# Optimization experiments

Hardware: AMD Instinct MI355X
Metric: run time of the kernel (lower is better)

## Reference

```python
import jax, jax.numpy as jnp
import numpy as np

B, L, D = 2048, 64, 128
NODES = 512
EPS = 1e-6


def setup_inputs() -> dict:
    key = jax.random.key(0)
    ks = jax.random.split(key, 9)
    src_ids = jax.random.randint(ks[0], (B, L), 0, NODES, dtype=jnp.int32)
    dst_ids = jax.random.randint(ks[1], (B, L), 0, NODES, dtype=jnp.int32)
    src_node_ids = jax.random.randint(ks[2], (B,), 1, NODES, dtype=jnp.int32)
    dst_node_ids = jax.random.randint(ks[3], (B,), 1, NODES, dtype=jnp.int32)
    node_interact_times = 100.0 + jax.random.uniform(ks[4], (B,), jnp.float32)
    src_times = jax.random.uniform(ks[5], (B, L), jnp.float32) * 100.0
    dst_times = jax.random.uniform(ks[6], (B, L), jnp.float32) * 100.0
    W1 = jax.random.normal(ks[7], (1, D), jnp.float32) * 0.5
    b1 = jnp.zeros((D,), jnp.float32)
    W2 = jax.random.normal(ks[8], (D, D), jnp.float32) * (1.0 / np.sqrt(D))
    b2 = jnp.zeros((D,), jnp.float32)
    return dict(src_padded_nodes_neighbor_ids=src_ids,
                dst_padded_nodes_neighbor_ids=dst_ids,
                src_node_ids=src_node_ids, dst_node_ids=dst_node_ids,
                node_interact_times=node_interact_times,
                src_padded_nodes_neighbor_times=src_times,
                dst_padded_nodes_neighbor_times=dst_times,
                W1=W1, b1=b1, W2=W2, b2=b2)


def _group_stats(ids, t):
    # per-position stats of the group sharing the same neighbor id. ids,t: (L,)
    n_pos = ids.shape[0]
    eq = ids[:, None] == ids[None, :]                       # (L,L) group membership
    n = eq.sum(1)                                           # group size at each position
    nf = n.astype(t.dtype)
    tb = jnp.broadcast_to(t[None, :], (n_pos, n_pos))
    tmax = jnp.max(jnp.where(eq, tb, -jnp.inf), axis=1)
    tmin = jnp.min(jnp.where(eq, tb, jnp.inf), axis=1)
    # mean(diff(sorted(ts))) == (max-min)/(n-1)
    avg_iat = jnp.where(n > 1, (tmax - tmin) / jnp.maximum(nf - 1.0, 1.0), 0.0)
    # stable rank of each element inside its own group (order statistic)
    pos = jnp.arange(n_pos)
    before = (t[:, None] < t[None, :]) | ((t[:, None] == t[None, :]) & (pos[:, None] < pos[None, :]))
    rank = jnp.sum(eq & before, axis=0)
    split = n // 2
    sel = eq & (rank[None, :] == split[:, None])            # exactly one per group
    t_split = jnp.sum(jnp.where(sel, tb, 0.0), axis=1)      # sorted(ts)[n//2]
    denom = jnp.maximum(nf - split.astype(t.dtype) - 1.0, 1.0)
    recent_iat = jnp.where(n >= 4, (tmax - t_split) / denom, 0.0)
    valid = ids != 0                                        # dicts skip neighbor id 0
    return nf, jnp.where(valid, avg_iat, 0.0), jnp.where(valid, recent_iat, 0.0)


def _cross_lookup(ids_a, ids_b, vals_b):
    # dict.get(nid, 0.0) over the other side's per-group values (id 0 excluded)
    match = (ids_a[:, None] == ids_b[None, :]) & (ids_b[None, :] != 0)
    idx = jnp.argmax(match, axis=1)
    return jnp.where(match.any(1), vals_b[idx], 0.0)


def _last_time(ids_a, ids_b, t_b):
    # dict comprehension keeps the LAST occurrence's timestamp (id 0 excluded)
    match = (ids_a[:, None] == ids_b[None, :]) & (ids_b[None, :] != 0)
    score = jnp.where(match, jnp.arange(ids_b.shape[0])[None, :], -1)
    li = score.max(1)
    return jnp.where(li >= 0, t_b[jnp.maximum(li, 0)], 0.0)


def _side_features(ids_a, t_a, ids_b, t_b, other_node_id, cur_t,
                   n_a, avg_a, rec_a, avg_b, rec_b, other_first):
    ft = t_a.dtype
    c_self = n_a
    c_other = jnp.sum(ids_a[:, None] == ids_b[None, :], axis=1).astype(ft)
    is_other = (ids_a == other_node_id).astype(ft)
    connects = (c_other > 0).astype(ft)
    freq_asym = jnp.where(c_other > 0, c_self / (c_other + EPS), 0.0)
    rcy_self = cur_t - t_a
    rcy_other = cur_t - _last_time(ids_a, ids_b, t_b)
    temp_asym = jnp.where(rcy_self > EPS, rcy_other / (rcy_self + EPS), 0.0)
    iat_other = _cross_lookup(ids_a, ids_b, avg_b)
    iat_asym = jnp.where(iat_other > EPS, avg_a / (iat_other + EPS), 0.0)
    riat_other = _cross_lookup(ids_a, ids_b, rec_b)
    riat_asym = jnp.where(riat_other > EPS, rec_a / (riat_other + EPS), 0.0)
    if other_first:
        head = [c_other, c_self]
    else:
        head = [c_self, c_other]
    return jnp.stack(head + [is_other, connects, freq_asym, temp_asym, iat_asym, riat_asym], axis=1)


def _per_sample(ids_s, ids_d, sid, did, cur_t, t_s, t_d):
    n_s, avg_s, rec_s = _group_stats(ids_s, t_s)
    n_d, avg_d, rec_d = _group_stats(ids_d, t_d)
    f_src = _side_features(ids_s, t_s, ids_d, t_d, did, cur_t,
                           n_s, avg_s, rec_s, avg_d, rec_d, False)
    f_dst = _side_features(ids_d, t_d, ids_s, t_s, sid, cur_t,
                           n_d, avg_d, rec_d, avg_s, rec_s, True)
    return f_src, f_dst


def _mlp_sum(feats, W1, b1, W2, b2):
    # Linear(1->D) -> ReLU -> Linear(D->D), applied per scalar feature, summed over the 8 features
    h = jax.nn.relu(feats[..., None] * W1[0] + b1)           # [B,L,8,D]
    y = jnp.einsum('blfd,de->blfe', h, W2) + b2
    return y.sum(axis=2)                                      # [B,L,D]


def reference(src_padded_nodes_neighbor_ids, dst_padded_nodes_neighbor_ids,
              src_node_ids, dst_node_ids, node_interact_times,
              src_padded_nodes_neighbor_times, dst_padded_nodes_neighbor_times,
              W1, b1, W2, b2):
    f_src, f_dst = jax.vmap(_per_sample)(
        src_padded_nodes_neighbor_ids, dst_padded_nodes_neighbor_ids,
        src_node_ids, dst_node_ids, node_interact_times,
        src_padded_nodes_neighbor_times, dst_padded_nodes_neighbor_times)
    f_src = jnp.where((src_padded_nodes_neighbor_ids == 0)[..., None], 0.0, f_src)
    f_dst = jnp.where((dst_padded_nodes_neighbor_ids == 0)[..., None], 0.0, f_dst)
    src_path_features = _mlp_sum(f_src, W1, b1, W2, b2)
    dst_path_features = _mlp_sum(f_dst, W1, b1, W2, b2)
    return src_path_features, dst_path_features
```

## Files before the change

### kernel.cpp

```cpp
#include <hip/hip_runtime.h>


#define EPSF 1e-6f
#define LDB 136

typedef __attribute__((ext_vector_type(8))) short bf16x8;
typedef __attribute__((ext_vector_type(4))) float f32x4;
typedef __attribute__((ext_vector_type(2))) float f32x2;

__device__ inline short f2bf(float x) {
    unsigned u = __float_as_uint(x);
    return (short)((u + 0x7fffu + ((u >> 16) & 1u)) >> 16);
}

__launch_bounds__(256, 2)
__global__ void lpe_fused4(const int* __restrict__ src_ids,
                           const int* __restrict__ dst_ids,
                           const int* __restrict__ src_nid,
                           const int* __restrict__ dst_nid,
                           const float* __restrict__ t_now,
                           const float* __restrict__ src_t,
                           const float* __restrict__ dst_t,
                           const float* __restrict__ W1,
                           const float* __restrict__ b1,
                           const float* __restrict__ W2,
                           const float* __restrict__ b2,
                           float* __restrict__ out)
{
    __shared__ int2  s_idt[128];
    __shared__ __align__(16) f32x4 s_tab[2][512];
    __shared__ float s_feats[128][9];
    __shared__ __align__(16) float s_w1[128], s_b1[128], s_b2[128];
    __shared__ __align__(16) float s_stage[4][32][32];
    __shared__ __align__(16) short W2T[128 * LDB];

    const int tid  = threadIdx.x;
    const int b4   = blockIdx.x * 4;
    const int lane = tid & 63, wv = tid >> 6;
    const int quad = lane >> 4, ln = lane & 15;
    const int side = (tid >> 6) & 1;
    const int i    = tid & 63;

    if (tid < 128) { s_w1[tid] = W1[tid]; s_b1[tid] = b1[tid]; s_b2[tid] = b2[tid]; }
    for (int u = tid; u < 16384; u += 256) {
        const int k = u >> 7, n = u & 127;
        W2T[n * LDB + k] = f2bf(W2[u]);
    }

    const int*   idp = side ? dst_ids : src_ids;
    const float* tp  = side ? dst_t   : src_t;

    int   pf_id = 0; float pf_t = 0.f;
    if (tid < 128) { pf_id = idp[b4 * 64 + i]; pf_t = tp[b4 * 64 + i]; }
    float cur = t_now[b4];
    int   s_n = src_nid[b4], d_n = dst_nid[b4];

    for (int u = tid; u < 1024; u += 256) ((float*)s_tab)[u * 4] = 0.f;

    const long side_stride = 2048L * 64L * 128L;

    for (int s = 0; s < 4; ++s) {
        const int   my_id = pf_id;  const float my_t = pf_t;
        const float curs  = cur;    const int sns = s_n, dns = d_n;
        if (tid < 128) s_idt[tid] = make_int2(my_id, __float_as_int(my_t));
        __syncthreads();

        float nf = 0.f, avg = 0.f;
        if (tid < 128) {
            int n = 0, rank = 0, later = 0;
            float tmax = -3.4e38f, tmin = 3.4e38f;
            const int sbase = side * 64;
            #pragma unroll 8
            for (int j = 0; j < 64; ++j) {
                const int2 e = s_idt[sbase + j];
                const float tj = __int_as_float(e.y);
                if (e.x == my_id) {
                    ++n;
                    tmax = fmaxf(tmax, tj);
                    tmin = fminf(tmin, tj);
                    if (tj < my_t || (tj == my_t && j < i)) ++rank;
                    if (j > i) later = 1;
                }
            }
            nf = (float)n;
            const int split = n >> 1;
            avg = (n > 1) ? (tmax - tmin) / (nf - 1.f) : 0.f;
            if (my_id != 0) {
                s_tab[side][my_id].x = nf;
                s_tab[side][my_id].y = avg;
                if (rank == split)
                    s_tab[side][my_id].z = (n >= 4)
                        ? (tmax - my_t) / fmaxf(nf - (float)split - 1.f, 1.f) : 0.f;
                if (!later)
                    s_tab[side][my_id].w = my_t;
            }
        }
        if (s < 3) {
            if (tid < 128) {
                pf_id = idp[(b4 + s + 1) * 64 + i];
                pf_t  = tp [(b4 + s + 1) * 64 + i];
            }
            cur = t_now[b4 + s + 1];
            s_n = src_nid[b4 + s + 1];
            d_n = dst_nid[b4 + s + 1];
        }
        __syncthreads();

        if (tid < 128) {
            const int os = side ^ 1;
            const float rec_m = (my_id != 0) ? s_tab[side][my_id].z : 0.f;
            const f32x4 to = s_tab[os][my_id];
            const float n_o = (my_id != 0) ? to.x : 0.f;
            const bool  hit = n_o > 0.f;
            const float avg_o = hit ? to.y : 0.f;
            const float rec_o = hit ? to.z : 0.f;
            const float lastt = hit ? to.w : 0.f;
            const int other_node = side ? sns : dns;
            const float m = (my_id != 0) ? 1.f : 0.f;

            const float rcy_s = curs - my_t;
            const float rcy_o = curs - lastt;
            s_feats[tid][0] = m * nf;
            s_feats[tid][1] = m * n_o;
            s_feats[tid][2] = m * ((my_id == other_node) ? 1.f : 0.f);
            s_feats[tid][3] = m * (hit ? 1.f : 0.f);
            s_feats[tid][4] = m * (hit ? nf / (n_o + EPSF) : 0.f);
            s_feats[tid][5] = m * ((rcy_s > EPSF) ? rcy_o / (rcy_s + EPSF) : 0.f);
            s_feats[tid][6] = m * ((avg_o > EPSF) ? avg / (avg_o + EPSF) : 0.f);
            s_feats[tid][7] = m * ((rec_o > EPSF) ? rec_m / (rec_o + EPSF) : 0.f);
        }
        __syncthreads();

        float fxr[2][8];
        #pragma unroll
        for (int rg = 0; rg < 2; ++rg) {
            const int row = wv * 32 + rg * 16 + ln;
            #pragma unroll
            for (int j = 0; j < 8; ++j) fxr[rg][j] = s_feats[row][j];
        }
        if (s < 3)
            for (int u = tid; u < 1024; u += 256) ((float*)s_tab)[u * 4] = 0.f;

        bf16x8 gf[2][4];
        #pragma unroll
        for (int kk = 0; kk < 4; ++kk) {
            const int kb = kk * 32 + quad * 8;
            #pragma unroll
            for (int rg = 0; rg < 2; ++rg) {
                #pragma unroll
                for (int u2 = 0; u2 < 4; ++u2) {
                    const f32x2 w  = *(const f32x2*)&s_w1[kb + u2 * 2];
                    const f32x2 bb = *(const f32x2*)&s_b1[kb + u2 * 2];
                    f32x2 sv = {0.f, 0.f};
                    #pragma unroll
                    for (int f = 0; f < 8; ++f) {
                        const f32x2 h = w * fxr[rg][f] + bb;
                        sv += __builtin_elementwise_max(h, (f32x2){0.f, 0.f});
                    }
                    gf[rg][kk][u2 * 2]     = f2bf(sv.x);
                    gf[rg][kk][u2 * 2 + 1] = f2bf(sv.y);
                }
            }
        }

        float* st = &s_stage[wv][0][0];
        const int sw = ln & 7;
        const long rowbase = (long)(b4 + s) * 64;

        #pragma unroll
        for (int p = 0; p < 4; ++p) {
            const int et0 = 2 * p, et1 = 2 * p + 1;
            bf16x8 afA[4], afB[4];
            #pragma unroll
            for (int kk = 0; kk < 4; ++kk) {
                afA[kk] = *(const bf16x8*)&W2T[(et0 * 16 + ln) * LDB + kk * 32 + quad * 8];
                afB[kk] = *(const bf16x8*)&W2T[(et1 * 16 + ln) * LDB + kk * 32 + quad * 8];
            }
            f32x4 accA[2] = {(f32x4){0.f,0.f,0.f,0.f}, (f32x4){0.f,0.f,0.f,0.f}};
            f32x4 accB[2] = {(f32x4){0.f,0.f,0.f,0.f}, (f32x4){0.f,0.f,0.f,0.f}};
            #pragma unroll
            for (int kk = 0; kk < 4; ++kk)
                #pragma unroll
                for (int rg = 0; rg < 2; ++rg) {
                    accA[rg] = __builtin_amdgcn_mfma_f32_16x16x32_bf16(afA[kk], gf[rg][kk], accA[rg], 0, 0, 0);
                    accB[rg] = __builtin_amdgcn_mfma_f32_16x16x32_bf16(afB[kk], gf[rg][kk], accB[rg], 0, 0, 0);
                }
            const f32x4 bA = *(const f32x4*)&s_b2[et0 * 16 + quad * 4] * 8.f;
            const f32x4 bB = *(const f32x4*)&s_b2[et1 * 16 + quad * 4] * 8.f;

            if (p)
                asm volatile("s_waitcnt lgkmcnt(0)" ::: "memory");
            #pragma unroll
            for (int rg = 0; rg < 2; ++rg) {
                const int row = rg * 16 + ln;
                *(f32x4*)&st[row * 32 + ((quad ^ sw) * 4)]       = accA[rg] + bA;
                *(f32x4*)&st[row * 32 + (((4 + quad) ^ sw) * 4)] = accB[rg] + bB;
            }
            asm volatile("s_waitcnt lgkmcnt(0)" ::: "memory");
            #pragma unroll
            for (int rr = 0; rr < 4; ++rr) {
                const int rl = rr * 8 + (lane >> 3);
                const f32x4 v = *(const f32x4*)&st[rl * 32 + (((lane & 7) ^ (rl & 7)) * 4)];
                const int row = wv * 32 + rl;
                const int sd = row >> 6, ii = row & 63;
                __builtin_nontemporal_store(v,
                    (f32x4*)&out[(long)sd * side_stride + (rowbase + ii) * 128
                                 + p * 32 + (lane & 7) * 4]);
            }
        }
    }
}

extern "C" void kernel_launch(void* const* d_in, const int* in_sizes, int n_in,
                              void* d_out, int out_size, void* d_ws, size_t ws_size,
                              hipStream_t stream) {
    (void)in_sizes; (void)n_in; (void)out_size; (void)d_ws; (void)ws_size;
    const int*   src_ids = (const int*)  d_in[0];
    const int*   dst_ids = (const int*)  d_in[1];
    const int*   src_nid = (const int*)  d_in[2];
    const int*   dst_nid = (const int*)  d_in[3];
    const float* t_now   = (const float*)d_in[4];
    const float* src_t   = (const float*)d_in[5];
    const float* dst_t   = (const float*)d_in[6];
    const float* W1      = (const float*)d_in[7];
    const float* b1      = (const float*)d_in[8];
    const float* W2      = (const float*)d_in[9];
    const float* b2      = (const float*)d_in[10];
    float* out = (float*)d_out;

    lpe_fused4<<<512, 256, 0, stream>>>(src_ids, dst_ids, src_nid, dst_nid,
                                        t_now, src_t, dst_t, W1, b1, W2, b2, out);
}
```

Before: 203.4 us.

## Split fused kernel into weight prep, feature, and GEMM kernels via workspace

```diff
diff --git a/kernel.cpp b/kernel.cpp
--- a/kernel.cpp
+++ b/kernel.cpp
@@ -11,6 +11,203 @@
 __device__ inline short f2bf(float x) {
     unsigned u = __float_as_uint(x);
     return (short)((u + 0x7fffu + ((u >> 16) & 1u)) >> 16);
+}
+
+__global__ void w2t_prep(const float* __restrict__ W2, short* __restrict__ w2t) {
+    const int idx = blockIdx.x * 256 + threadIdx.x;
+    const int k = idx >> 7, n = idx & 127;
+    w2t[n * 128 + k] = f2bf(W2[idx]);
+}
+
+__launch_bounds__(128)
+__global__ void lpe_feats(const int* __restrict__ src_ids,
+                          const int* __restrict__ dst_ids,
+                          const int* __restrict__ src_nid,
+                          const int* __restrict__ dst_nid,
+                          const float* __restrict__ t_now,
+                          const float* __restrict__ src_t,
+                          const float* __restrict__ dst_t,
+                          float* __restrict__ fs)
+{
+    __shared__ int2  s_idt[128];
+    __shared__ __align__(16) f32x4 s_tab[2][512];
+
+    const int tid  = threadIdx.x;
+    const int b    = blockIdx.x;
+    const int side = tid >> 6;
+    const int i    = tid & 63;
+
+    #pragma unroll
+    for (int u = tid; u < 1024; u += 128) ((float*)s_tab)[u * 4] = 0.f;
+
+    const float cur = t_now[b];
+    const int   s_n = src_nid[b], d_n = dst_nid[b];
+
+    const int*   idp = side ? dst_ids : src_ids;
+    const float* tp  = side ? dst_t   : src_t;
+    const int   my_id = idp[b * 64 + i];
+    const float my_t  = tp [b * 64 + i];
+    s_idt[tid] = make_int2(my_id, __float_as_int(my_t));
+    __syncthreads();
+
+    int n = 0, rank = 0, later = 0;
+    float tmax = -3.4e38f, tmin = 3.4e38f;
+    const int sbase = side * 64;
+    #pragma unroll 8
+    for (int j = 0; j < 64; ++j) {
+        const int2 e = s_idt[sbase + j];
+        const float tj = __int_as_float(e.y);
+        if (e.x == my_id) {
+            ++n;
+            tmax = fmaxf(tmax, tj);
+            tmin = fminf(tmin, tj);
+            if (tj < my_t || (tj == my_t && j < i)) ++rank;
+            if (j > i) later = 1;
+        }
+    }
+    const float nf    = (float)n;
+    const int   split = n >> 1;
+    const float avg   = (n > 1) ? (tmax - tmin) / (nf - 1.f) : 0.f;
+    if (my_id != 0) {
+        s_tab[side][my_id].x = nf;
+        s_tab[side][my_id].y = avg;
+        if (rank == split)
+            s_tab[side][my_id].z = (n >= 4)
+                ? (tmax - my_t) / fmaxf(nf - (float)split - 1.f, 1.f) : 0.f;
+        if (!later)
+            s_tab[side][my_id].w = my_t;
+    }
+    __syncthreads();
+
+    const int os = side ^ 1;
+    const float rec_m = (my_id != 0) ? s_tab[side][my_id].z : 0.f;
+    const f32x4 to = s_tab[os][my_id];
+    const float n_o = (my_id != 0) ? to.x : 0.f;
+    const bool  hit = n_o > 0.f;
+    const float avg_o = hit ? to.y : 0.f;
+    const float rec_o = hit ? to.z : 0.f;
+    const float lastt = hit ? to.w : 0.f;
+    const int other_node = side ? s_n : d_n;
+    const float m = (my_id != 0) ? 1.f : 0.f;
+
+    const float rcy_s = cur - my_t;
+    const float rcy_o = cur - lastt;
+    f32x4 f0, f1;
+    f0.x = m * nf;
+    f0.y = m * n_o;
+    f0.z = m * ((my_id == other_node) ? 1.f : 0.f);
+    f0.w = m * (hit ? 1.f : 0.f);
+    f1.x = m * (hit ? nf / (n_o + EPSF) : 0.f);
+    f1.y = m * ((rcy_s > EPSF) ? rcy_o / (rcy_s + EPSF) : 0.f);
+    f1.z = m * ((avg_o > EPSF) ? avg / (avg_o + EPSF) : 0.f);
+    f1.w = m * ((rec_o > EPSF) ? rec_m / (rec_o + EPSF) : 0.f);
+
+    const long rowf = (long)side * 131072 + (long)b * 64 + i;
+    *(f32x4*)&fs[rowf * 8]     = f0;
+    *(f32x4*)&fs[rowf * 8 + 4] = f1;
+}
+
+__launch_bounds__(256, 3)
+__global__ void lpe_gemm(const float* __restrict__ fs,
+                         const short* __restrict__ w2t,
+                         const float* __restrict__ W1,
+                         const float* __restrict__ b1,
+                         const float* __restrict__ b2,
+                         float* __restrict__ out)
+{
+    __shared__ __align__(16) float s_w1[128], s_b1[128], s_b2[128];
+    __shared__ __align__(16) short W2T[128 * LDB];
+    __shared__ __align__(16) float s_stage[4][32][32];
+
+    const int tid  = threadIdx.x;
+    const int lane = tid & 63, wv = tid >> 6;
+    const int quad = lane >> 4, ln = lane & 15;
+
+    #pragma unroll
+    for (int it = 0; it < 8; ++it) {
+        const int c = tid + it * 256;
+        const int n = c >> 4, j = c & 15;
+        *(bf16x8*)&W2T[n * LDB + j * 8] = *(const bf16x8*)&w2t[n * 128 + j * 8];
+    }
+    if (tid < 128) { s_w1[tid] = W1[tid]; s_b1[tid] = b1[tid]; s_b2[tid] = b2[tid]; }
+    __syncthreads();
+
+    const long base = (long)blockIdx.x * 128;
+
+    float fxr[2][8];
+    #pragma unroll
+    for (int rg = 0; rg < 2; ++rg) {
+        const long rowf = base + wv * 32 + rg * 16 + ln;
+        const f32x4 a = *(const f32x4*)&fs[rowf * 8];
+        const f32x4 c = *(const f32x4*)&fs[rowf * 8 + 4];
+        fxr[rg][0] = a.x; fxr[rg][1] = a.y; fxr[rg][2] = a.z; fxr[rg][3] = a.w;
+        fxr[rg][4] = c.x; fxr[rg][5] = c.y; fxr[rg][6] = c.z; fxr[rg][7] = c.w;
+    }
+
+    bf16x8 gf[2][4];
+    #pragma unroll
+    for (int kk = 0; kk < 4; ++kk) {
+        const int kb = kk * 32 + quad * 8;
+        #pragma unroll
+        for (int rg = 0; rg < 2; ++rg) {
+            #pragma unroll
+            for (int u2 = 0; u2 < 4; ++u2) {
+                const f32x2 w  = *(const f32x2*)&s_w1[kb + u2 * 2];
+                const f32x2 bb = *(const f32x2*)&s_b1[kb + u2 * 2];
+                f32x2 sv = {0.f, 0.f};
+                #pragma unroll
+                for (int f = 0; f < 8; ++f) {
+                    const f32x2 h = w * fxr[rg][f] + bb;
+                    sv += __builtin_elementwise_max(h, (f32x2){0.f, 0.f});
+                }
+                gf[rg][kk][u2 * 2]     = f2bf(sv.x);
+                gf[rg][kk][u2 * 2 + 1] = f2bf(sv.y);
+            }
+        }
+    }
+
+    float* st = &s_stage[wv][0][0];
+    const int sw = ln & 7;
+
+    #pragma unroll
+    for (int p = 0; p < 4; ++p) {
+        const int et0 = 2 * p, et1 = 2 * p + 1;
+        bf16x8 afA[4], afB[4];
+        #pragma unroll
+        for (int kk = 0; kk < 4; ++kk) {
+            afA[kk] = *(const bf16x8*)&W2T[(et0 * 16 + ln) * LDB + kk * 32 + quad * 8];
+            afB[kk] = *(const bf16x8*)&W2T[(et1 * 16 + ln) * LDB + kk * 32 + quad * 8];
+        }
+        f32x4 accA[2] = {(f32x4){0.f,0.f,0.f,0.f}, (f32x4){0.f,0.f,0.f,0.f}};
+        f32x4 accB[2] = {(f32x4){0.f,0.f,0.f,0.f}, (f32x4){0.f,0.f,0.f,0.f}};
+        #pragma unroll
+        for (int kk = 0; kk < 4; ++kk)
+            #pragma unroll
+            for (int rg = 0; rg < 2; ++rg) {
+                accA[rg] = __builtin_amdgcn_mfma_f32_16x16x32_bf16(afA[kk], gf[rg][kk], accA[rg], 0, 0, 0);
+                accB[rg] = __builtin_amdgcn_mfma_f32_16x16x32_bf16(afB[kk], gf[rg][kk], accB[rg], 0, 0, 0);
+            }
+        const f32x4 bA = *(const f32x4*)&s_b2[et0 * 16 + quad * 4] * 8.f;
+        const f32x4 bB = *(const f32x4*)&s_b2[et1 * 16 + quad * 4] * 8.f;
+
+        if (p)
+            asm volatile("s_waitcnt lgkmcnt(0)" ::: "memory");
+        #pragma unroll
+        for (int rg = 0; rg < 2; ++rg) {
+            const int row = rg * 16 + ln;
+            *(f32x4*)&st[row * 32 + ((quad ^ sw) * 4)]       = accA[rg] + bA;
+            *(f32x4*)&st[row * 32 + (((4 + quad) ^ sw) * 4)] = accB[rg] + bB;
+        }
+        asm volatile("s_waitcnt lgkmcnt(0)" ::: "memory");
+        #pragma unroll
+        for (int rr = 0; rr < 4; ++rr) {
+            const int rl = rr * 8 + (lane >> 3);
+            const f32x4 v = *(const f32x4*)&st[rl * 32 + (((lane & 7) ^ (rl & 7)) * 4)];
+            const long rowf = base + wv * 32 + rl;
+            __builtin_nontemporal_store(v,
+                (f32x4*)&out[rowf * 128 + p * 32 + (lane & 7) * 4]);
+        }
+    }
 }
 
 __launch_bounds__(256, 2)
@@ -46,17 +243,13 @@
         const int k = u >> 7, n = u & 127;
         W2T[n * LDB + k] = f2bf(W2[u]);
     }
-
     const int*   idp = side ? dst_ids : src_ids;
     const float* tp  = side ? dst_t   : src_t;
-
     int   pf_id = 0; float pf_t = 0.f;
     if (tid < 128) { pf_id = idp[b4 * 64 + i]; pf_t = tp[b4 * 64 + i]; }
     float cur = t_now[b4];
     int   s_n = src_nid[b4], d_n = dst_nid[b4];
-
     for (int u = tid; u < 1024; u += 256) ((float*)s_tab)[u * 4] = 0.f;
-
     const long side_stride = 2048L * 64L * 128L;
 
     for (int s = 0; s < 4; ++s) {
@@ -75,9 +268,7 @@
                 const int2 e = s_idt[sbase + j];
                 const float tj = __int_as_float(e.y);
                 if (e.x == my_id) {
-                    ++n;
-                    tmax = fmaxf(tmax, tj);
-                    tmin = fminf(tmin, tj);
+                    ++n; tmax = fmaxf(tmax, tj); tmin = fminf(tmin, tj);
                     if (tj < my_t || (tj == my_t && j < i)) ++rank;
                     if (j > i) later = 1;
                 }
@@ -91,8 +282,7 @@
                 if (rank == split)
                     s_tab[side][my_id].z = (n >= 4)
                         ? (tmax - my_t) / fmaxf(nf - (float)split - 1.f, 1.f) : 0.f;
-                if (!later)
-                    s_tab[side][my_id].w = my_t;
+                if (!later) s_tab[side][my_id].w = my_t;
             }
         }
         if (s < 3) {
@@ -117,7 +307,6 @@
             const float lastt = hit ? to.w : 0.f;
             const int other_node = side ? sns : dns;
             const float m = (my_id != 0) ? 1.f : 0.f;
-
             const float rcy_s = curs - my_t;
             const float rcy_o = curs - lastt;
             s_feats[tid][0] = m * nf;
@@ -214,7 +403,7 @@
 extern "C" void kernel_launch(void* const* d_in, const int* in_sizes, int n_in,
                               void* d_out, int out_size, void* d_ws, size_t ws_size,
                               hipStream_t stream) {
-    (void)in_sizes; (void)n_in; (void)out_size; (void)d_ws; (void)ws_size;
+    (void)in_sizes; (void)n_in; (void)out_size;
     const int*   src_ids = (const int*)  d_in[0];
     const int*   dst_ids = (const int*)  d_in[1];
     const int*   src_nid = (const int*)  d_in[2];
@@ -228,6 +417,18 @@
     const float* b2      = (const float*)d_in[10];
     float* out = (float*)d_out;
 
-    lpe_fused4<<<512, 256, 0, stream>>>(src_ids, dst_ids, src_nid, dst_nid,
-                                        t_now, src_t, dst_t, W1, b1, W2, b2, out);
-}
+    const size_t W2T_BYTES  = 128 * 128 * sizeof(short);
+    const size_t FEAT_BYTES = 262144ULL * 8 * sizeof(float);
+
+    if (ws_size >= W2T_BYTES + FEAT_BYTES) {
+        short* w2t = (short*)d_ws;
+        float* fs  = (float*)((char*)d_ws + W2T_BYTES);
+        w2t_prep<<<64, 256, 0, stream>>>(W2, w2t);
+        lpe_feats<<<2048, 128, 0, stream>>>(src_ids, dst_ids, src_nid, dst_nid,
+                                            t_now, src_t, dst_t, fs);
+        lpe_gemm<<<2048, 256, 0, stream>>>(fs, w2t, W1, b1, b2, out);
+    } else {
+        lpe_fused4<<<512, 256, 0, stream>>>(src_ids, dst_ids, src_nid, dst_nid,
+                                            t_now, src_t, dst_t, W1, b1, W2, b2, out);
+    }
+}
```

New measurement: 185.3 us. 1.1x faster.
